# Performance work log

Hardware: AMD Instinct MI355X
Metric: run time of the kernel (lower is better)

## Reference

```python
import jax, jax.numpy as jnp
import numpy as np

MAX_ITER = 3  # matches init kwarg max_iter


def setup_inputs() -> dict:
    key = jax.random.key(0)
    k1, k2, k3, k4 = jax.random.split(key, 4)
    B, S = 4, 160
    return {
        "s_edge": jax.random.normal(k1, (B, S, S), dtype=jnp.float32),
        "s_sib": jax.random.normal(k2, (B, S, S, S), dtype=jnp.float32),
        "s_cop": jax.random.normal(k3, (B, S, S, S), dtype=jnp.float32),
        "s_grd": jax.random.normal(k4, (B, S, S, S), dtype=jnp.float32),
        "mask": jnp.ones((B, S, S), dtype=bool),
    }


def reference(s_edge, s_sib, s_cop, s_grd, mask):
    B, S, _ = mask.shape
    idx = jnp.arange(S)
    # Permute to the [head, mod, (sib), batch] layout used by the torch code.
    mask_p = jnp.transpose(mask, (2, 1, 0))              # [h, m, B]
    # 2nd-order mask: both (h,m) and (h,t) arcs valid, and t != h, t != m
    pair_ok = mask_p[:, None, :, :] & mask_p[:, :, None, :]   # [h, m, t, B]
    t_ok = (idx[:, None, None] != idx[None, None, :]) & (
        idx[None, :, None] != idx[None, None, :])             # [h, m, t]
    mask2o = (pair_ok & t_ok[..., None]).astype(s_edge.dtype)  # [h, m, t, B]

    se = jnp.transpose(s_edge, (2, 1, 0))                 # [h, m, B]
    ss = jnp.transpose(s_sib, (2, 1, 3, 0)) * mask2o      # [h, m, t, B]
    sc = jnp.transpose(s_cop, (2, 1, 3, 0)) * mask2o
    sg = jnp.transpose(s_grd, (2, 1, 3, 0)) * mask2o

    q = jnp.zeros((2, S, S, B), dtype=se.dtype)
    for _ in range(MAX_ITER):
        q1 = jax.nn.softmax(q, axis=0)[1]                 # [h, m, B]
        # f[h,m,b] = sum_t q1[h,t,b]*ss + q1[t,m,b]*sc + q1[m,t,b]*sg
        f = (jnp.einsum('htb,hmtb->hmb', q1, ss)
             + jnp.einsum('tmb,hmtb->hmb', q1, sc)
             + jnp.einsum('mtb,hmtb->hmb', q1, sg))
        q = jnp.stack([jnp.zeros_like(f), se + f])        # [2, h, m, B]

    logQ = jax.nn.log_softmax(jnp.transpose(q, (3, 2, 1, 0)), axis=-1)  # [B, m, h... -> B,S,S,2]
    return jnp.exp(logQ)
```

## Files before the change

kernel.cpp:

```cpp
#include <hip/hip_runtime.h>
#include <cmath>

constexpr int S = 160;
constexpr int BATCH = 4;
constexpr int ZSPLIT = 2;
constexpr int ROWS = S / ZSPLIT;
constexpr int KC = S / 4;
constexpr int TPB = 256;
constexpr int LPR = 8;
constexpr int CPL = KC / LPR;
constexpr int RPP = TPB / LPR;
constexpr int PASSES = (ROWS + RPP - 1) / RPP;

__device__ __forceinline__ float sigmoidf_(float x) {
  return 1.0f / (1.0f + expf(-x));
}

__global__ void prep_wf(const int* __restrict__ mask, unsigned char* __restrict__ wf) {
  int i = blockIdx.x * blockDim.x + threadIdx.x;
  if (i >= BATCH * S * S) return;
  int t = i % S;
  int bh = i / S;
  int h = bh % S;
  int b = bh / S;
  wf[i] = (mask[(b * S + t) * S + h] != 0 && t != h) ? 1 : 0;
}

template <bool FIRST, bool LAST>
__global__ __launch_bounds__(TPB, 4) void mfvi_iter(
    const float* __restrict__ s_edge,
    const float* __restrict__ s_sib,
    const float* __restrict__ s_cop,
    const float* __restrict__ s_grd,
    const int* __restrict__ mask,
    const unsigned char* __restrict__ wf,
    const float* __restrict__ q1_in,
    float* __restrict__ q1_out,
    float* __restrict__ outp) {
  const int m = blockIdx.x;
  const int b = blockIdx.y;
  const int z = blockIdx.z;
  const int tid = threadIdx.x;

  __shared__ __align__(16) float colm[S];
  __shared__ __align__(16) float rowm[S];
  __shared__ float sef[ROWS];
  __shared__ float pmf[ROWS];

  const float* G = q1_in + (size_t)b * S * S;
  const size_t bm = (size_t)b * S + m;
  const int h0 = z * ROWS;

  if (tid < S) {
    if (!FIRST) {
      colm[tid] = G[tid * S + m];
      rowm[tid] = G[m * S + tid];
    }
    if (tid < ROWS) {
      sef[tid] = s_edge[bm * S + h0 + tid];
      pmf[tid] = (mask[bm * S + h0 + tid] != 0) ? 1.0f : 0.0f;
    }
  }
  __syncthreads();

  const size_t blk = (bm * S + h0) * (size_t)S;
  const float4* SS = (const float4*)(s_sib + blk);
  const float4* CC = (const float4*)(s_cop + blk);
  const float4* GG = (const float4*)(s_grd + blk);
  const float4* QQ = (const float4*)(G + h0 * S);
  const unsigned* WF = (const unsigned*)(wf + ((size_t)b * S + h0) * S);
  const int msel = m >> 2;
  const unsigned mclr = ~(255u << ((m & 3) * 8));

  const int g = tid >> 3;
  const int j = tid & 7;

#pragma unroll
  for (int p = 0; p < PASSES; ++p) {
    const int r = p * RPP + g;
    if (r < ROWS) {
      const int rowbase = r * KC;
      float acc = 0.0f;
#pragma unroll
      for (int i = 0; i < CPL; ++i) {
        const int k = j + i * LPR;
        const int c = rowbase + k;
        unsigned wu = WF[c];
        float4 s = SS[c];
        float4 cv = CC[c];
        float4 gv = GG[c];
        if (k == msel) wu &= mclr;
        float w0 = (float)(wu & 255u);
        float w1 = (float)((wu >> 8) & 255u);
        float w2 = (float)((wu >> 16) & 255u);
        float w3 = (float)(wu >> 24);
        if (FIRST) {
          float t0 = s.x + cv.x + gv.x;
          float t1 = s.y + cv.y + gv.y;
          float t2 = s.z + cv.z + gv.z;
          float t3 = s.w + cv.w + gv.w;
          acc = fmaf(w0, t0, fmaf(w1, t1, fmaf(w2, t2, fmaf(w3, t3, acc))));
        } else {
          float4 q = QQ[c];
          float4 cm = ((const float4*)colm)[k];
          float4 rm = ((const float4*)rowm)[k];
          float t0 = fmaf(q.x, s.x, fmaf(cm.x, cv.x, rm.x * gv.x));
          float t1 = fmaf(q.y, s.y, fmaf(cm.y, cv.y, rm.y * gv.y));
          float t2 = fmaf(q.z, s.z, fmaf(cm.z, cv.z, rm.z * gv.z));
          float t3 = fmaf(q.w, s.w, fmaf(cm.w, cv.w, rm.w * gv.w));
          acc = fmaf(w0, t0, fmaf(w1, t1, fmaf(w2, t2, fmaf(w3, t3, acc))));
        }
      }
      acc += __shfl_xor(acc, 1);
      acc += __shfl_xor(acc, 2);
      acc += __shfl_xor(acc, 4);
      if (j == 0) {
        const int h = h0 + r;
        const float qv = fmaf(pmf[r], FIRST ? 0.5f * acc : acc, sef[r]);
        if (!LAST) {
          q1_out[((size_t)b * S + h) * S + m] = sigmoidf_(qv);
        } else {
          float2 o;
          o.x = sigmoidf_(-qv);
          o.y = sigmoidf_(qv);
          ((float2*)outp)[bm * S + h] = o;
        }
      }
    }
  }
}

extern "C" void kernel_launch(void* const* d_in, const int* in_sizes, int n_in,
                              void* d_out, int out_size, void* d_ws, size_t ws_size,
                              hipStream_t stream) {
  const float* s_edge = (const float*)d_in[0];
  const float* s_sib = (const float*)d_in[1];
  const float* s_cop = (const float*)d_in[2];
  const float* s_grd = (const float*)d_in[3];
  const int* mask = (const int*)d_in[4];
  float* outp = (float*)d_out;

  const int qn = BATCH * S * S;
  float* q1A = (float*)d_ws;
  float* q1B = q1A + qn;
  unsigned char* wf = (unsigned char*)(q1B + qn);

  prep_wf<<<(qn + 255) / 256, 256, 0, stream>>>(mask, wf);

  dim3 grid(S, BATCH, ZSPLIT);
  mfvi_iter<true, false><<<grid, TPB, 0, stream>>>(
      s_edge, s_sib, s_cop, s_grd, mask, wf, q1A, q1B, nullptr);
  mfvi_iter<false, false><<<grid, TPB, 0, stream>>>(
      s_edge, s_sib, s_cop, s_grd, mask, wf, q1B, q1A, nullptr);
  mfvi_iter<false, true><<<grid, TPB, 0, stream>>>(
      s_edge, s_sib, s_cop, s_grd, mask, wf, q1A, nullptr, outp);
}
```

Before: 263.3 us.

## Precompute masked fp16 score tensors once and reuse in later iterations

The first iteration now writes masked, pre-weighted copies of the sibling, coparent and grandparent scores in fp16 to workspace. The later iterations read these half-size arrays instead of three fp32 tensors plus the mask, using a finer row split. It also keeps a transposed copy of q1 so the column load is contiguous. Extra write traffic and fp16 rounding error are the trade-offs, and the path only runs if the workspace is large enough.

```diff
diff --git a/kernel.cpp b/kernel.cpp
--- a/kernel.cpp
+++ b/kernel.cpp
@@ -1,16 +1,23 @@
 #include <hip/hip_runtime.h>
 #include <cmath>
 
+typedef _Float16 hf;
+typedef hf hf4 __attribute__((ext_vector_type(4)));
+
 constexpr int S = 160;
 constexpr int BATCH = 4;
+constexpr int KC = S / 4;
+constexpr int TPB = 256;
+
 constexpr int ZSPLIT = 2;
 constexpr int ROWS = S / ZSPLIT;
-constexpr int KC = S / 4;
-constexpr int TPB = 256;
 constexpr int LPR = 8;
 constexpr int CPL = KC / LPR;
 constexpr int RPP = TPB / LPR;
 constexpr int PASSES = (ROWS + RPP - 1) / RPP;
+
+constexpr int ZC = 5;
+constexpr int CROWS = S / ZC;
 
 __device__ __forceinline__ float sigmoidf_(float x) {
   return 1.0f / (1.0f + expf(-x));
@@ -26,16 +33,168 @@
   wf[i] = (mask[(b * S + t) * S + h] != 0 && t != h) ? 1 : 0;
 }
 
-template <bool FIRST, bool LAST>
-__global__ __launch_bounds__(TPB, 4) void mfvi_iter(
+__global__ __launch_bounds__(TPB, 4) void mfvi_first(
     const float* __restrict__ s_edge,
     const float* __restrict__ s_sib,
     const float* __restrict__ s_cop,
     const float* __restrict__ s_grd,
     const int* __restrict__ mask,
     const unsigned char* __restrict__ wf,
+    hf* __restrict__ Aw, hf* __restrict__ Bw, hf* __restrict__ Cw,
+    float* __restrict__ q1_out,
+    float* __restrict__ q1t_out) {
+  const int m = blockIdx.x;
+  const int b = blockIdx.y;
+  const int z = blockIdx.z;
+  const int tid = threadIdx.x;
+
+  __shared__ float sef[ROWS];
+  __shared__ float pmf[ROWS];
+
+  const size_t bm = (size_t)b * S + m;
+  const int h0 = z * ROWS;
+
+  if (tid < ROWS) {
+    sef[tid] = s_edge[bm * S + h0 + tid];
+    pmf[tid] = (mask[bm * S + h0 + tid] != 0) ? 1.0f : 0.0f;
+  }
+  __syncthreads();
+
+  const size_t blk = (bm * S + h0) * (size_t)S;
+  const float4* SS = (const float4*)(s_sib + blk);
+  const float4* CC = (const float4*)(s_cop + blk);
+  const float4* GG = (const float4*)(s_grd + blk);
+  const unsigned* WF = (const unsigned*)(wf + ((size_t)b * S + h0) * S);
+  hf* A16 = Aw + blk;
+  hf* B16 = Bw + blk;
+  hf* C16 = Cw + blk;
+  const int msel = m >> 2;
+  const unsigned mclr = ~(255u << ((m & 3) * 8));
+
+  const int g = tid >> 3;
+  const int j = tid & 7;
+
+#pragma unroll
+  for (int p = 0; p < PASSES; ++p) {
+    const int r = p * RPP + g;
+    if (r < ROWS) {
+      const float pm = pmf[r];
+      float acc = 0.0f;
+#pragma unroll
+      for (int i = 0; i < CPL; ++i) {
+        const int k = j + i * LPR;
+        const int c = r * KC + k;
+        unsigned wu = WF[c];
+        float4 s = SS[c];
+        float4 cv = CC[c];
+        float4 gv = GG[c];
+        if (k == msel) wu &= mclr;
+        const float w0 = (float)(wu & 255u) * pm;
+        const float w1 = (float)((wu >> 8) & 255u) * pm;
+        const float w2 = (float)((wu >> 16) & 255u) * pm;
+        const float w3 = (float)(wu >> 24) * pm;
+        const float a0 = w0 * s.x, a1 = w1 * s.y, a2 = w2 * s.z, a3 = w3 * s.w;
+        const float b0 = w0 * cv.x, b1 = w1 * cv.y, b2 = w2 * cv.z, b3 = w3 * cv.w;
+        const float c0 = w0 * gv.x, c1 = w1 * gv.y, c2 = w2 * gv.z, c3 = w3 * gv.w;
+        acc += ((a0 + b0 + c0) + (a1 + b1 + c1)) +
+               ((a2 + b2 + c2) + (a3 + b3 + c3));
+        hf4 av = {(hf)a0, (hf)a1, (hf)a2, (hf)a3};
+        hf4 bv = {(hf)b0, (hf)b1, (hf)b2, (hf)b3};
+        hf4 cw = {(hf)c0, (hf)c1, (hf)c2, (hf)c3};
+        *(hf4*)(A16 + 4 * c) = av;
+        *(hf4*)(B16 + 4 * c) = bv;
+        *(hf4*)(C16 + 4 * c) = cw;
+      }
+      acc += __shfl_xor(acc, 1);
+      acc += __shfl_xor(acc, 2);
+      acc += __shfl_xor(acc, 4);
+      if (j == 0) {
+        const int h = h0 + r;
+        const float qv = fmaf(0.5f, acc, sef[r]);
+        const float sg1 = sigmoidf_(qv);
+        q1_out[((size_t)b * S + h) * S + m] = sg1;
+        q1t_out[bm * S + h] = sg1;
+      }
+    }
+  }
+}
+
+template <bool LAST>
+__global__ __launch_bounds__(TPB, 4) void mfvi_next(
+    const float* __restrict__ s_edge,
+    const hf* __restrict__ Aw, const hf* __restrict__ Bw, const hf* __restrict__ Cw,
     const float* __restrict__ q1_in,
-    float* __restrict__ q1_out,
+    const float* __restrict__ q1t_in,
+    float* __restrict__ q1_out, float* __restrict__ q1t_out,
+    float* __restrict__ outp) {
+  const int m = blockIdx.x;
+  const int b = blockIdx.y;
+  const int z = blockIdx.z;
+  const int tid = threadIdx.x;
+
+  __shared__ __align__(16) float colm[S];
+  __shared__ __align__(16) float rowm[S];
+  __shared__ float sef[CROWS];
+
+  const size_t bm = (size_t)b * S + m;
+  const int h0 = z * CROWS;
+
+  if (tid < S) {
+    colm[tid] = q1t_in[bm * S + tid];
+    rowm[tid] = q1_in[bm * S + tid];
+    if (tid < CROWS) sef[tid] = s_edge[bm * S + h0 + tid];
+  }
+  __syncthreads();
+
+  const size_t blk = (bm * S + h0) * (size_t)S;
+  const hf* A16 = Aw + blk;
+  const hf* B16 = Bw + blk;
+  const hf* C16 = Cw + blk;
+  const float4* QQ = (const float4*)(q1_in + (size_t)b * S * S + (size_t)h0 * S);
+
+  const int r = tid >> 3;
+  const int j = tid & 7;
+  float acc = 0.0f;
+#pragma unroll
+  for (int i = 0; i < CPL; ++i) {
+    const int k = j + i * LPR;
+    const int c = r * KC + k;
+    hf4 a = *(const hf4*)(A16 + 4 * c);
+    hf4 bv = *(const hf4*)(B16 + 4 * c);
+    hf4 g = *(const hf4*)(C16 + 4 * c);
+    float4 q = QQ[c];
+    float4 cm = ((const float4*)colm)[k];
+    float4 rm = ((const float4*)rowm)[k];
+    acc = fmaf(q.x, (float)a.x, fmaf(cm.x, (float)bv.x, fmaf(rm.x, (float)g.x, acc)));
+    acc = fmaf(q.y, (float)a.y, fmaf(cm.y, (float)bv.y, fmaf(rm.y, (float)g.y, acc)));
+    acc = fmaf(q.z, (float)a.z, fmaf(cm.z, (float)bv.z, fmaf(rm.z, (float)g.z, acc)));
+    acc = fmaf(q.w, (float)a.w, fmaf(cm.w, (float)bv.w, fmaf(rm.w, (float)g.w, acc)));
+  }
+  acc += __shfl_xor(acc, 1);
+  acc += __shfl_xor(acc, 2);
+  acc += __shfl_xor(acc, 4);
+  if (j == 0) {
+    const int h = h0 + r;
+    const float qv = sef[r] + acc;
+    if (!LAST) {
+      const float sg1 = sigmoidf_(qv);
+      q1_out[((size_t)b * S + h) * S + m] = sg1;
+      q1t_out[bm * S + h] = sg1;
+    } else {
+      float2 o;
+      o.x = sigmoidf_(-qv);
+      o.y = sigmoidf_(qv);
+      ((float2*)outp)[bm * S + h] = o;
+    }
+  }
+}
+
+template <bool FIRST, bool LAST>
+__global__ __launch_bounds__(TPB, 4) void mfvi_iter(
+    const float* __restrict__ s_edge, const float* __restrict__ s_sib,
+    const float* __restrict__ s_cop, const float* __restrict__ s_grd,
+    const int* __restrict__ mask, const unsigned char* __restrict__ wf,
+    const float* __restrict__ q1_in, float* __restrict__ q1_out,
     float* __restrict__ outp) {
   const int m = blockIdx.x;
   const int b = blockIdx.y;
@@ -141,17 +300,43 @@
   float* outp = (float*)d_out;
 
   const int qn = BATCH * S * S;
-  float* q1A = (float*)d_ws;
-  float* q1B = q1A + qn;
-  unsigned char* wf = (unsigned char*)(q1B + qn);
-
-  prep_wf<<<(qn + 255) / 256, 256, 0, stream>>>(mask, wf);
-
-  dim3 grid(S, BATCH, ZSPLIT);
-  mfvi_iter<true, false><<<grid, TPB, 0, stream>>>(
-      s_edge, s_sib, s_cop, s_grd, mask, wf, q1A, q1B, nullptr);
-  mfvi_iter<false, false><<<grid, TPB, 0, stream>>>(
-      s_edge, s_sib, s_cop, s_grd, mask, wf, q1B, q1A, nullptr);
-  mfvi_iter<false, true><<<grid, TPB, 0, stream>>>(
-      s_edge, s_sib, s_cop, s_grd, mask, wf, q1A, nullptr, outp);
-}
+  const size_t NS3 = (size_t)BATCH * S * S * S;
+  const size_t need = 3 * NS3 * sizeof(hf) + 4 * (size_t)qn * sizeof(float) + qn;
+
+  if (ws_size >= need) {
+    hf* Aw = (hf*)d_ws;
+    hf* Bw = Aw + NS3;
+    hf* Cw = Bw + NS3;
+    float* q1B = (float*)(Cw + NS3);
+    float* q1Bt = q1B + qn;
+    float* q1A = q1Bt + qn;
+    float* q1At = q1A + qn;
+    unsigned char* wf = (unsigned char*)(q1At + qn);
+
+    prep_wf<<<(qn + 255) / 256, 256, 0, stream>>>(mask, wf);
+
+    dim3 gridP(S, BATCH, ZSPLIT);
+    mfvi_first<<<gridP, TPB, 0, stream>>>(
+        s_edge, s_sib, s_cop, s_grd, mask, wf, Aw, Bw, Cw, q1B, q1Bt);
+
+    dim3 gridC(S, BATCH, ZC);
+    mfvi_next<false><<<gridC, TPB, 0, stream>>>(
+        s_edge, Aw, Bw, Cw, q1B, q1Bt, q1A, q1At, nullptr);
+    mfvi_next<true><<<gridC, TPB, 0, stream>>>(
+        s_edge, Aw, Bw, Cw, q1A, q1At, nullptr, nullptr, outp);
+  } else {
+    float* q1A = (float*)d_ws;
+    float* q1B = q1A + qn;
+    unsigned char* wf = (unsigned char*)(q1B + qn);
+
+    prep_wf<<<(qn + 255) / 256, 256, 0, stream>>>(mask, wf);
+
+    dim3 grid(S, BATCH, ZSPLIT);
+    mfvi_iter<true, false><<<grid, TPB, 0, stream>>>(
+        s_edge, s_sib, s_cop, s_grd, mask, wf, q1A, q1B, nullptr);
+    mfvi_iter<false, false><<<grid, TPB, 0, stream>>>(
+        s_edge, s_sib, s_cop, s_grd, mask, wf, q1B, q1A, nullptr);
+    mfvi_iter<false, true><<<grid, TPB, 0, stream>>>(
+        s_edge, s_sib, s_cop, s_grd, mask, wf, q1A, nullptr, outp);
+  }
+}
```

New measurement: 261.8 us. No clear change (-0.6%).

## Cache masked scores as fp16 in workspace for later MFVI iterations

Applied to the files above, without the earlier changes.

The first iteration now reads the three fp32 score tensors once, applies the mask and writes masked copies in fp16 to workspace. Iterations two and three read only this half-size buffer. The kernel also keeps a transposed copy of q1 so the column gather turns into a contiguous load. This is meant to cut HBM traffic in the later iterations, at the cost of an extra fp16 write pass, reduced precision in the scores, and a fallback to the old path when the workspace is too small.

```diff
diff --git a/kernel.cpp b/kernel.cpp
--- a/kernel.cpp
+++ b/kernel.cpp
@@ -1,16 +1,27 @@
 #include <hip/hip_runtime.h>
 #include <cmath>
 
+typedef _Float16 hf;
+typedef hf hf8 __attribute__((ext_vector_type(8)));
+
 constexpr int S = 160;
 constexpr int BATCH = 4;
-constexpr int ZSPLIT = 2;
-constexpr int ROWS = S / ZSPLIT;
-constexpr int KC = S / 4;
 constexpr int TPB = 256;
-constexpr int LPR = 8;
-constexpr int CPL = KC / LPR;
+
+constexpr int KC8 = S / 8;
+constexpr int LPR = 4;
+constexpr int CPL = KC8 / LPR;
 constexpr int RPP = TPB / LPR;
-constexpr int PASSES = (ROWS + RPP - 1) / RPP;
+constexpr int NZ = 3;
+constexpr int XROW = 3 * S;
+
+constexpr int FZSPLIT = 2;
+constexpr int FROWS = S / FZSPLIT;
+constexpr int FKC = S / 4;
+constexpr int FLPR = 8;
+constexpr int FCPL = FKC / FLPR;
+constexpr int FRPP = TPB / FLPR;
+constexpr int FPASSES = (FROWS + FRPP - 1) / FRPP;
 
 __device__ __forceinline__ float sigmoidf_(float x) {
   return 1.0f / (1.0f + expf(-x));
@@ -26,16 +37,102 @@
   wf[i] = (mask[(b * S + t) * S + h] != 0 && t != h) ? 1 : 0;
 }
 
-template <bool FIRST, bool LAST>
-__global__ __launch_bounds__(TPB, 4) void mfvi_iter(
+__global__ __launch_bounds__(TPB, 4) void mfvi_first(
     const float* __restrict__ s_edge,
     const float* __restrict__ s_sib,
     const float* __restrict__ s_cop,
     const float* __restrict__ s_grd,
     const int* __restrict__ mask,
     const unsigned char* __restrict__ wf,
+    hf* __restrict__ X,
+    float* __restrict__ q1_out,
+    float* __restrict__ q1t_out) {
+  const int m = blockIdx.x;
+  const int b = blockIdx.y;
+  const int z = blockIdx.z;
+  const int tid = threadIdx.x;
+
+  __shared__ float sef[RPP];
+  __shared__ float pmf[RPP];
+
+  const size_t bm = (size_t)b * S + m;
+  const int h0 = z * RPP;
+  const int nrows = (h0 + RPP <= S) ? RPP : (S - h0);
+
+  if (tid < nrows) {
+    sef[tid] = s_edge[bm * S + h0 + tid];
+    pmf[tid] = (mask[bm * S + h0 + tid] != 0) ? 1.0f : 0.0f;
+  }
+  __syncthreads();
+
+  const int r = tid >> 2;
+  const int j = tid & 3;
+  if (r >= nrows) return;
+  const int h = h0 + r;
+
+  const size_t rowf = (bm * S + h) * (size_t)S;
+  const float4* SSr = (const float4*)(s_sib + rowf);
+  const float4* CCr = (const float4*)(s_cop + rowf);
+  const float4* GGr = (const float4*)(s_grd + rowf);
+  const uint2* WFr = (const uint2*)(wf + ((size_t)b * S + h) * S);
+  hf* Xr = X + (bm * S + h) * (size_t)XROW;
+
+  const int msel8 = m >> 3;
+  const unsigned mclr = ~(255u << ((m & 3) * 8));
+  const float pm = pmf[r];
+
+  float acc = 0.0f;
+#pragma unroll
+  for (int i = 0; i < CPL; ++i) {
+    const int c = j + i * LPR;
+    uint2 wu = WFr[c];
+    float4 s0 = SSr[2 * c], s1 = SSr[2 * c + 1];
+    float4 c0 = CCr[2 * c], c1 = CCr[2 * c + 1];
+    float4 g0 = GGr[2 * c], g1 = GGr[2 * c + 1];
+    if (c == msel8) { if (m & 4) wu.y &= mclr; else wu.x &= mclr; }
+    const float w0 = (float)(wu.x & 255u) * pm;
+    const float w1 = (float)((wu.x >> 8) & 255u) * pm;
+    const float w2 = (float)((wu.x >> 16) & 255u) * pm;
+    const float w3 = (float)(wu.x >> 24) * pm;
+    const float w4 = (float)(wu.y & 255u) * pm;
+    const float w5 = (float)((wu.y >> 8) & 255u) * pm;
+    const float w6 = (float)((wu.y >> 16) & 255u) * pm;
+    const float w7 = (float)(wu.y >> 24) * pm;
+
+    const float a0 = w0 * s0.x, a1 = w1 * s0.y, a2 = w2 * s0.z, a3 = w3 * s0.w;
+    const float a4 = w4 * s1.x, a5 = w5 * s1.y, a6 = w6 * s1.z, a7 = w7 * s1.w;
+    const float b0 = w0 * c0.x, b1 = w1 * c0.y, b2 = w2 * c0.z, b3 = w3 * c0.w;
+    const float b4 = w4 * c1.x, b5 = w5 * c1.y, b6 = w6 * c1.z, b7 = w7 * c1.w;
+    const float e0 = w0 * g0.x, e1 = w1 * g0.y, e2 = w2 * g0.z, e3 = w3 * g0.w;
+    const float e4 = w4 * g1.x, e5 = w5 * g1.y, e6 = w6 * g1.z, e7 = w7 * g1.w;
+
+    acc += ((a0 + b0 + e0) + (a1 + b1 + e1)) + ((a2 + b2 + e2) + (a3 + b3 + e3)) +
+           ((a4 + b4 + e4) + (a5 + b5 + e5)) + ((a6 + b6 + e6) + (a7 + b7 + e7));
+
+    hf8 A = {(hf)a0, (hf)a1, (hf)a2, (hf)a3, (hf)a4, (hf)a5, (hf)a6, (hf)a7};
+    hf8 B = {(hf)b0, (hf)b1, (hf)b2, (hf)b3, (hf)b4, (hf)b5, (hf)b6, (hf)b7};
+    hf8 C = {(hf)e0, (hf)e1, (hf)e2, (hf)e3, (hf)e4, (hf)e5, (hf)e6, (hf)e7};
+    *(hf8*)(Xr + 8 * c) = A;
+    *(hf8*)(Xr + S + 8 * c) = B;
+    *(hf8*)(Xr + 2 * S + 8 * c) = C;
+  }
+  acc += __shfl_xor(acc, 1);
+  acc += __shfl_xor(acc, 2);
+  if (j == 0) {
+    const float qv = fmaf(0.5f, acc, sef[r]);
+    const float sg1 = sigmoidf_(qv);
+    q1_out[((size_t)b * S + h) * S + m] = sg1;
+    q1t_out[bm * S + h] = sg1;
+  }
+}
+
+template <bool LAST>
+__global__ __launch_bounds__(TPB, 4) void mfvi_next(
+    const float* __restrict__ s_edge,
+    const hf* __restrict__ X,
     const float* __restrict__ q1_in,
-    float* __restrict__ q1_out,
+    const float* __restrict__ q1t_in,
+    float* __restrict__ q1_out, float* __restrict__ q1t_out,
     float* __restrict__ outp) {
   const int m = blockIdx.x;
   const int b = blockIdx.y;
@@ -44,19 +141,92 @@
 
   __shared__ __align__(16) float colm[S];
   __shared__ __align__(16) float rowm[S];
-  __shared__ float sef[ROWS];
-  __shared__ float pmf[ROWS];
+  __shared__ float sef[RPP];
+
+  const size_t bm = (size_t)b * S + m;
+  const int h0 = z * RPP;
+  const int nrows = (h0 + RPP <= S) ? RPP : (S - h0);
+
+  if (tid < S) {
+    colm[tid] = q1t_in[bm * S + tid];
+    rowm[tid] = q1_in[bm * S + tid];
+    if (tid < nrows) sef[tid] = s_edge[bm * S + h0 + tid];
+  }
+  __syncthreads();
+
+  const int r = tid >> 2;
+  const int j = tid & 3;
+  if (r >= nrows) return;
+  const int h = h0 + r;
+
+  const hf* Ar = X + (bm * S + h) * (size_t)XROW;
+  const hf* Br = Ar + S;
+  const hf* Cr = Ar + 2 * S;
+  const float4* Qr = (const float4*)(q1_in + ((size_t)b * S + h) * (size_t)S);
+
+  float acc = 0.0f;
+#pragma unroll
+  for (int i = 0; i < CPL; ++i) {
+    const int c = j + i * LPR;
+    hf8 A = *(const hf8*)(Ar + 8 * c);
+    hf8 B = *(const hf8*)(Br + 8 * c);
+    hf8 C = *(const hf8*)(Cr + 8 * c);
+    float4 q0 = Qr[2 * c], q1v = Qr[2 * c + 1];
+    float4 cm0 = ((const float4*)colm)[2 * c], cm1 = ((const float4*)colm)[2 * c + 1];
+    float4 rm0 = ((const float4*)rowm)[2 * c], rm1 = ((const float4*)rowm)[2 * c + 1];
+    acc = fmaf(q0.x, (float)A[0], fmaf(cm0.x, (float)B[0], fmaf(rm0.x, (float)C[0], acc)));
+    acc = fmaf(q0.y, (float)A[1], fmaf(cm0.y, (float)B[1], fmaf(rm0.y, (float)C[1], acc)));
+    acc = fmaf(q0.z, (float)A[2], fmaf(cm0.z, (float)B[2], fmaf(rm0.z, (float)C[2], acc)));
+    acc = fmaf(q0.w, (float)A[3], fmaf(cm0.w, (float)B[3], fmaf(rm0.w, (float)C[3], acc)));
+    acc = fmaf(q1v.x, (float)A[4], fmaf(cm1.x, (float)B[4], fmaf(rm1.x, (float)C[4], acc)));
+    acc = fmaf(q1v.y, (float)A[5], fmaf(cm1.y, (float)B[5], fmaf(rm1.y, (float)C[5], acc)));
+    acc = fmaf(q1v.z, (float)A[6], fmaf(cm1.z, (float)B[6], fmaf(rm1.z, (float)C[6], acc)));
+    acc = fmaf(q1v.w, (float)A[7], fmaf(cm1.w, (float)B[7], fmaf(rm1.w, (float)C[7], acc)));
+  }
+  acc += __shfl_xor(acc, 1);
+  acc += __shfl_xor(acc, 2);
+  if (j == 0) {
+    const float qv = sef[r] + acc;
+    if (!LAST) {
+      const float sg1 = sigmoidf_(qv);
+      q1_out[((size_t)b * S + h) * S + m] = sg1;
+      q1t_out[bm * S + h] = sg1;
+    } else {
+      float2 o;
+      o.x = sigmoidf_(-qv);
+      o.y = sigmoidf_(qv);
+      ((float2*)outp)[bm * S + h] = o;
+    }
+  }
+}
+
+template <bool FIRST, bool LAST>
+__global__ __launch_bounds__(TPB, 4) void mfvi_iter(
+    const float* __restrict__ s_edge, const float* __restrict__ s_sib,
+    const float* __restrict__ s_cop, const float* __restrict__ s_grd,
+    const int* __restrict__ mask, const unsigned char* __restrict__ wf,
+    const float* __restrict__ q1_in, float* __restrict__ q1_out,
+    float* __restrict__ outp) {
+  const int m = blockIdx.x;
+  const int b = blockIdx.y;
+  const int z = blockIdx.z;
+  const int tid = threadIdx.x;
+
+  __shared__ __align__(16) float colm[S];
+  __shared__ __align__(16) float rowm[S];
+  __shared__ float sef[FROWS];
+  __shared__ float pmf[FROWS];
 
   const float* G = q1_in + (size_t)b * S * S;
   const size_t bm = (size_t)b * S + m;
-  const int h0 = z * ROWS;
+  const int h0 = z * FROWS;
 
   if (tid < S) {
     if (!FIRST) {
       colm[tid] = G[tid * S + m];
       rowm[tid] = G[m * S + tid];
     }
-    if (tid < ROWS) {
+    if (tid < FROWS) {
       sef[tid] = s_edge[bm * S + h0 + tid];
       pmf[tid] = (mask[bm * S + h0 + tid] != 0) ? 1.0f : 0.0f;
     }
@@ -76,14 +246,14 @@
   const int j = tid & 7;
 
 #pragma unroll
-  for (int p = 0; p < PASSES; ++p) {
-    const int r = p * RPP + g;
-    if (r < ROWS) {
-      const int rowbase = r * KC;
+  for (int p = 0; p < FPASSES; ++p) {
+    const int r = p * FRPP + g;
+    if (r < FROWS) {
+      const int rowbase = r * FKC;
       float acc = 0.0f;
 #pragma unroll
-      for (int i = 0; i < CPL; ++i) {
-        const int k = j + i * LPR;
+      for (int i = 0; i < FCPL; ++i) {
+        const int k = j + i * FLPR;
         const int c = rowbase + k;
         unsigned wu = WF[c];
         float4 s = SS[c];
@@ -141,17 +311,39 @@
   float* outp = (float*)d_out;
 
   const int qn = BATCH * S * S;
-  float* q1A = (float*)d_ws;
-  float* q1B = q1A + qn;
-  unsigned char* wf = (unsigned char*)(q1B + qn);
-
-  prep_wf<<<(qn + 255) / 256, 256, 0, stream>>>(mask, wf);
-
-  dim3 grid(S, BATCH, ZSPLIT);
-  mfvi_iter<true, false><<<grid, TPB, 0, stream>>>(
-      s_edge, s_sib, s_cop, s_grd, mask, wf, q1A, q1B, nullptr);
-  mfvi_iter<false, false><<<grid, TPB, 0, stream>>>(
-      s_edge, s_sib, s_cop, s_grd, mask, wf, q1B, q1A, nullptr);
-  mfvi_iter<false, true><<<grid, TPB, 0, stream>>>(
-      s_edge, s_sib, s_cop, s_grd, mask, wf, q1A, nullptr, outp);
-}
+  const size_t NS3 = (size_t)BATCH * S * S * S;
+  const size_t need = 3 * NS3 * sizeof(hf) + 4 * (size_t)qn * sizeof(float) + qn;
+
+  if (ws_size >= need) {
+    hf* X = (hf*)d_ws;
+    float* q1B = (float*)(X + 3 * NS3);
+    float* q1Bt = q1B + qn;
+    float* q1A = q1Bt + qn;
+    float* q1At = q1A + qn;
+    unsigned char* wf = (unsigned char*)(q1At + qn);
+
+    prep_wf<<<(qn + 255) / 256, 256, 0, stream>>>(mask, wf);
+
+    dim3 grid(S, BATCH, NZ);
+    mfvi_first<<<grid, TPB, 0, stream>>>(
+        s_edge, s_sib, s_cop, s_grd, mask, wf, X, q1B, q1Bt);
+    mfvi_next<false><<<grid, TPB, 0, stream>>>(
+        s_edge, X, q1B, q1Bt, q1A, q1At, nullptr);
+    mfvi_next<true><<<grid, TPB, 0, stream>>>(
+        s_edge, X, q1A, q1At, nullptr, nullptr, outp);
+  } else {
+    float* q1A = (float*)d_ws;
+    float* q1B = q1A + qn;
+    unsigned char* wf = (unsigned char*)(q1B + qn);
+
+    prep_wf<<<(qn + 255) / 256, 256, 0, stream>>>(mask, wf);
+
+    dim3 grid(S, BATCH, FZSPLIT);
+    mfvi_iter<true, false><<<grid, TPB, 0, stream>>>(
+        s_edge, s_sib, s_cop, s_grd, mask, wf, q1A, q1B, nullptr);
+    mfvi_iter<false, false><<<grid, TPB, 0, stream>>>(
+        s_edge, s_sib, s_cop, s_grd, mask, wf, q1B, q1A, nullptr);
+    mfvi_iter<false, true><<<grid, TPB, 0, stream>>>(
+        s_edge, s_sib, s_cop, s_grd, mask, wf, q1A, nullptr, outp);
+  }
+}
```

After: 282.7 us. 1.07x slower.
